# Kernel tuning notes

Hardware: AMD Instinct MI355X
Metric: run time of the kernel (lower is better)

Reference implementation:

```python
import jax, jax.numpy as jnp
import numpy as np

B, C, H, W = 64, 64, 64, 64
KD = 64  # kernel_dim == res == dim (required by the torch reshapes)


def _ln(t, g, b, eps=1e-5):
    mu = jnp.mean(t, axis=-1, keepdims=True)
    var = jnp.var(t, axis=-1, keepdims=True)
    return (t - mu) * jax.lax.rsqrt(var + eps) * g + b


def _cos_map(n, kd):
    i = jnp.arange(n, dtype=jnp.float32)[:, None]
    j = jnp.arange(kd, dtype=jnp.float32)[None, :]
    return jnp.cos(i * j * jnp.pi / n) / kd


def setup_inputs() -> dict:
    key = jax.random.key(0)
    ks = jax.random.split(key, 6)
    s = 0.02
    return {
        "x": jax.random.normal(ks[0], (B, C, H, W), jnp.float32),
        "freq_embed": jax.random.normal(ks[1], (H, W, C), jnp.float32),
        "g_k": jnp.ones((C,), jnp.float32), "b_k": jnp.zeros((C,), jnp.float32),
        "Wk": jax.random.normal(ks[2], (C, KD), jnp.float32) * s, "bk": jnp.zeros((KD,), jnp.float32),
        "g_z": jnp.ones((C,), jnp.float32), "b_z": jnp.zeros((C,), jnp.float32),
        "Wz": jax.random.normal(ks[3], (C, C), jnp.float32) * s, "bz": jnp.zeros((C,), jnp.float32),
        "g_o": jnp.ones((KD,), jnp.float32), "b_o": jnp.zeros((KD,), jnp.float32),
        "Wo": jax.random.normal(ks[4], (KD, C), jnp.float32) * s, "bo": jnp.zeros((C,), jnp.float32),
    }


def reference(x, freq_embed, g_k, b_k, Wk, bk, g_z, b_z, Wz, bz, g_o, b_o, Wo, bo):
    # x: (B,C,H,W) -> (B,H,W,C), matching the torch permute branch
    x = jnp.transpose(x, (0, 2, 3, 1))
    Bc, Hc, Wc, Cc = x.shape
    kd = Wk.shape[1]
    xin = x + freq_embed[None]                    # freq_embed broadcast over batch
    k = _ln(xin, g_k, b_k) @ Wk + bk              # (B,H,W,kd)
    z = _ln(freq_embed, g_z, b_z) @ Wz + bz       # to_k(freq_embed): (H,W,C)
    cosn = _cos_map(Hc, kd)                       # (H,kd)
    cosm = _cos_map(Wc, kd)                       # (W,kd)
    i = jnp.arange(Hc, dtype=jnp.float32)[:, None]
    j = jnp.arange(Wc, dtype=jnp.float32)[None, :]
    decay = (jnp.exp(-(i + j) / max(Hc, Wc)) / kd).astype(x.dtype)  # (H,W)
    wexp = decay[:, :, None] ** z                 # (H,W,C), decay > 0
    # separable forward DCT (two kernel-1 conv1d == two contractions)
    t = jnp.einsum('nh,bhwc->bnwc', cosn, k)
    t = jnp.einsum('mw,bnwc->bnmc', cosm, t)
    t = t * wexp[None]                            # exponential-decay spectral gate
    # separable inverse DCT
    t = jnp.einsum('nh,bnmc->bhmc', cosn, t)
    t = jnp.einsum('mw,bhmc->bhwc', cosm, t)
    out = _ln(t, g_o, b_o) * jax.nn.silu(z)[None]
    out = out @ Wo + bo
    return jnp.transpose(out, (0, 3, 1, 2))       # back to BCHW
```

## Files before the change

### kernel.cpp

```cpp
#include <hip/hip_runtime.h>


typedef __attribute__((ext_vector_type(8))) short short8;
typedef __attribute__((ext_vector_type(4))) float f32x4;
typedef __attribute__((ext_vector_type(4))) unsigned short us4;

__device__ __forceinline__ unsigned short bfhi(float f) {
    return (unsigned short)(__builtin_bit_cast(unsigned int, f) >> 16);
}
__device__ __forceinline__ float hif(float f) {
    return __builtin_bit_cast(float, __builtin_bit_cast(unsigned int, f) & 0xFFFF0000u);
}
__device__ __forceinline__ int swa(int row, int col) {
    return (row << 7) + (((col >> 3) ^ (row & 7)) << 4) + ((col & 7) << 1);
}
__device__ __forceinline__ short8 fragrd(const short* buf, int row, int kc) {
    int a = (row << 7) + ((kc ^ (row & 7)) << 4);
    return *(const short8*)((const char*)buf + a);
}

__device__ __forceinline__ void mm_block(const short* Ah, const short* Al,
                                         const short* Bh, const short* Bl,
                                         int m0, int n0, int l15, int q,
                                         f32x4 (&acc)[2][2]) {
    const f32x4 zero = {0.f, 0.f, 0.f, 0.f};
    acc[0][0] = zero; acc[0][1] = zero; acc[1][0] = zero; acc[1][1] = zero;
    #pragma unroll
    for (int kb = 0; kb < 2; ++kb) {
        int kc = (kb << 2) + q;
        short8 a0h = fragrd(Ah, m0 + l15, kc);
        short8 a0l = fragrd(Al, m0 + l15, kc);
        short8 a1h = fragrd(Ah, m0 + 16 + l15, kc);
        short8 a1l = fragrd(Al, m0 + 16 + l15, kc);
        short8 b0h = fragrd(Bh, n0 + l15, kc);
        short8 b0l = fragrd(Bl, n0 + l15, kc);
        short8 b1h = fragrd(Bh, n0 + 16 + l15, kc);
        short8 b1l = fragrd(Bl, n0 + 16 + l15, kc);
        acc[0][0] = __builtin_amdgcn_mfma_f32_16x16x32_bf16(a0h, b0h, acc[0][0], 0, 0, 0);
        acc[0][0] = __builtin_amdgcn_mfma_f32_16x16x32_bf16(a0h, b0l, acc[0][0], 0, 0, 0);
        acc[0][0] = __builtin_amdgcn_mfma_f32_16x16x32_bf16(a0l, b0h, acc[0][0], 0, 0, 0);
        acc[0][1] = __builtin_amdgcn_mfma_f32_16x16x32_bf16(a0h, b1h, acc[0][1], 0, 0, 0);
        acc[0][1] = __builtin_amdgcn_mfma_f32_16x16x32_bf16(a0h, b1l, acc[0][1], 0, 0, 0);
        acc[0][1] = __builtin_amdgcn_mfma_f32_16x16x32_bf16(a0l, b1h, acc[0][1], 0, 0, 0);
        acc[1][0] = __builtin_amdgcn_mfma_f32_16x16x32_bf16(a1h, b0h, acc[1][0], 0, 0, 0);
        acc[1][0] = __builtin_amdgcn_mfma_f32_16x16x32_bf16(a1h, b0l, acc[1][0], 0, 0, 0);
        acc[1][0] = __builtin_amdgcn_mfma_f32_16x16x32_bf16(a1l, b0h, acc[1][0], 0, 0, 0);
        acc[1][1] = __builtin_amdgcn_mfma_f32_16x16x32_bf16(a1h, b1h, acc[1][1], 0, 0, 0);
        acc[1][1] = __builtin_amdgcn_mfma_f32_16x16x32_bf16(a1h, b1l, acc[1][1], 0, 0, 0);
        acc[1][1] = __builtin_amdgcn_mfma_f32_16x16x32_bf16(a1l, b1h, acc[1][1], 0, 0, 0);
    }
}

__global__ __launch_bounds__(256) void k_pre1(
    const float* __restrict__ g_k, const float* __restrict__ b_k,
    const float* __restrict__ Wk, const float* __restrict__ bk,
    const float* __restrict__ g_z, const float* __restrict__ b_z,
    const float* __restrict__ Wz, const float* __restrict__ bz,
    const float* __restrict__ Wo,
    unsigned short* __restrict__ WkTh, unsigned short* __restrict__ WkTl,
    float* __restrict__ su_k, float* __restrict__ v_k,
    unsigned short* __restrict__ WzTh, unsigned short* __restrict__ WzTl,
    float* __restrict__ su_z, float* __restrict__ v_z,
    unsigned short* __restrict__ WoTh, unsigned short* __restrict__ WoTl,
    unsigned short* __restrict__ cos_hi, unsigned short* __restrict__ cos_lo) {
    int t = threadIdx.x;
    if (blockIdx.x < 16) {
        int n = blockIdx.x * 4 + (t >> 6);
        int c = t & 63;
        float wk = Wk[c * 64 + n];
        float a = g_k[c] * wk;
        WkTh[n * 64 + c] = bfhi(a);
        WkTl[n * 64 + c] = bfhi(a - hif(a));
        float sa = a, sv = b_k[c] * wk;
        #pragma unroll
        for (int off = 32; off > 0; off >>= 1) {
            sa += __shfl_xor(sa, off, 64);
            sv += __shfl_xor(sv, off, 64);
        }
        if (c == 0) { su_k[n] = sa; v_k[n] = sv + bk[n]; }
        float wz = Wz[c * 64 + n];
        float az = g_z[c] * wz;
        WzTh[n * 64 + c] = bfhi(az);
        WzTl[n * 64 + c] = bfhi(az - hif(az));
        float saz = az, svz = b_z[c] * wz;
        #pragma unroll
        for (int off = 32; off > 0; off >>= 1) {
            saz += __shfl_xor(saz, off, 64);
            svz += __shfl_xor(svz, off, 64);
        }
        if (c == 0) { su_z[n] = saz; v_z[n] = svz + bz[n]; }
        float wo = Wo[c * 64 + n];
        WoTh[n * 64 + c] = bfhi(wo);
        WoTl[n * 64 + c] = bfhi(wo - hif(wo));
    } else {
        int idx = (blockIdx.x - 16) * 256 + t;
        int i = idx >> 6, j = idx & 63;
        float ang = (float)(i * j) * 3.14159265358979323846f * (1.0f / 64.0f);
        float v = cosf(ang) * (1.0f / 64.0f);
        cos_hi[idx] = bfhi(v);
        cos_lo[idx] = bfhi(v - hif(v));
    }
}

__global__ __launch_bounds__(256) void k_pre2(
    const float* __restrict__ freq,
    const unsigned short* __restrict__ WzTh_g, const unsigned short* __restrict__ WzTl_g,
    const float* __restrict__ su_z, const float* __restrict__ v_z,
    float* __restrict__ siluzT, float* __restrict__ wexpT,
    float* __restrict__ freqT) {
    __shared__ short Ah[4096], Al[4096], Bh[4096], Bl[4096];
    __shared__ float muS[64], rsS[64];
    __shared__ float tile[64][65];
    int t = threadIdx.x;
    if (blockIdx.x < 64) {
        int h = blockIdx.x;
        #pragma unroll
        for (int p = 0; p < 2; ++p) {
            int e = t + p * 256;
            int row = e >> 3, ch = e & 7;
            int a = (row << 7) + (((ch ^ (row & 7)) << 4));
            *(uint4*)((char*)Bh + a) = *(const uint4*)&WzTh_g[row * 64 + ch * 8];
            *(uint4*)((char*)Bl + a) = *(const uint4*)&WzTl_g[row * 64 + ch * 8];
        }
        int w = t >> 2, c0 = (t & 3) << 4;
        float4 fr[4];
        float s1 = 0.f, s2 = 0.f;
        #pragma unroll
        for (int i = 0; i < 4; ++i) {
            fr[i] = *(const float4*)&freq[(h * 64 + w) * 64 + c0 + 4 * i];
            s1 += fr[i].x + fr[i].y + fr[i].z + fr[i].w;
            s2 += fr[i].x * fr[i].x + fr[i].y * fr[i].y + fr[i].z * fr[i].z + fr[i].w * fr[i].w;
        }
        s1 += __shfl_xor(s1, 1, 64); s1 += __shfl_xor(s1, 2, 64);
        s2 += __shfl_xor(s2, 1, 64); s2 += __shfl_xor(s2, 2, 64);
        float mu = s1 * (1.0f / 64.0f);
        float var = s2 * (1.0f / 64.0f) - mu * mu;
        float rs = rsqrtf(var + 1e-5f);
        if ((t & 3) == 0) { muS[w] = mu; rsS[w] = rs; }
        const float* fp = (const float*)fr;
        #pragma unroll
        for (int i = 0; i < 4; ++i) {
            us4 hv, lv;
            #pragma unroll
            for (int r = 0; r < 4; ++r) {
                float f = fp[i * 4 + r];
                hv[r] = bfhi(f);
                lv[r] = bfhi(f - hif(f));
            }
            int a = swa(w, c0 + 4 * i);
            *(us4*)((char*)Ah + a) = hv;
            *(us4*)((char*)Al + a) = lv;
        }
        __syncthreads();
        int lane = t & 63, wv = t >> 6;
        int q = lane >> 4, l15 = lane & 15;
        int m0 = (wv & 1) << 5, n0 = (wv >> 1) << 5;
        f32x4 acc[2][2];
        mm_block(Ah, Al, Bh, Bl, m0, n0, l15, q, acc);
        #pragma unroll
        for (int u = 0; u < 2; ++u) {
            int c = n0 + (u << 4) + l15;
            float suc = su_z[c], vc = v_z[c];
            #pragma unroll
            for (int ti = 0; ti < 2; ++ti) {
                int wb = m0 + (ti << 4) + (q << 2);
                float4 mu4 = *(const float4*)&muS[wb];
                float4 rs4 = *(const float4*)&rsS[wb];
                float4 sil, wx;
                #pragma unroll
                for (int r = 0; r < 4; ++r) {
                    float z = ((const float*)&rs4)[r] * (acc[ti][u][r] - ((const float*)&mu4)[r] * suc) + vc;
                    float lnd = -(float)(h + wb + r) * 0.015625f - 4.1588830833596718565f;
                    ((float*)&sil)[r] = z / (1.0f + expf(-z));
                    ((float*)&wx)[r] = expf(z * lnd);
                }
                int base = (c * 64 + h) * 64 + wb;
                *(float4*)&siluzT[base] = sil;
                *(float4*)&wexpT[base] = wx;
            }
        }
    } else {
        int h = blockIdx.x - 64;
        int w = t >> 2, c0 = (t & 3) << 4;
        #pragma unroll
        for (int i = 0; i < 4; ++i)
            *(float4*)&tile[w][c0 + 4 * i] = *(const float4*)&freq[(h * 64 + w) * 64 + c0 + 4 * i];
        __syncthreads();
        int w0 = (t & 15) << 2;
        #pragma unroll
        for (int p = 0; p < 4; ++p) {
            int c = (t >> 4) + 16 * p;
            float4 fv = make_float4(tile[w0][c], tile[w0 + 1][c], tile[w0 + 2][c], tile[w0 + 3][c]);
            *(float4*)&freqT[(c * 64 + h) * 64 + w0] = fv;
        }
    }
}

__global__ __launch_bounds__(256, 3) void k_k(
    const float* __restrict__ x, const float* __restrict__ freqT,
    const unsigned short* __restrict__ WkTh_g, const unsigned short* __restrict__ WkTl_g,
    const float* __restrict__ su_k, const float* __restrict__ v_k,
    float* __restrict__ planes) {
    __shared__ short Ah[4096], Al[4096], Bh[4096], Bl[4096];
    __shared__ __align__(16) float red1[16][68], red2[16][68];
    __shared__ float muS[64], rsS[64];
    int b = blockIdx.x >> 6, h = blockIdx.x & 63;
    int t = threadIdx.x;
    #pragma unroll
    for (int p = 0; p < 2; ++p) {
        int e = t + p * 256;
        int row = e >> 3, ch = e & 7;
        int a = (row << 7) + (((ch ^ (row & 7)) << 4));
        *(uint4*)((char*)Bh + a) = *(const uint4*)&WkTh_g[row * 64 + ch * 8];
        *(uint4*)((char*)Bl + a) = *(const uint4*)&WkTl_g[row * 64 + ch * 8];
    }
    int g = t >> 4, w0 = (t & 15) << 2, c0 = g << 2;
    const float* xb = x + (size_t)b * 262144 + h * 64;
    float4 vr[4];
    float4 s1 = {0,0,0,0}, s2 = {0,0,0,0};
    #pragma unroll
    for (int i = 0; i < 4; ++i) {
        int c = c0 + i;
        float4 xv = *(const float4*)&xb[c * 4096 + w0];
        float4 fv = *(const float4*)&freqT[c * 4096 + h * 64 + w0];
        xv.x += fv.x; xv.y += fv.y; xv.z += fv.z; xv.w += fv.w;
        vr[i] = xv;
        s1.x += xv.x; s1.y += xv.y; s1.z += xv.z; s1.w += xv.w;
        s2.x += xv.x * xv.x; s2.y += xv.y * xv.y; s2.z += xv.z * xv.z; s2.w += xv.w * xv.w;
    }
    const float* vp = (const float*)vr;
    #pragma unroll
    for (int j = 0; j < 4; ++j) {
        us4 hv, lv;
        #pragma unroll
        for (int r = 0; r < 4; ++r) {
            float f = vp[r * 4 + j];
            hv[r] = bfhi(f);
            lv[r] = bfhi(f - hif(f));
        }
        int a = swa(w0 + j, c0);
        *(us4*)((char*)Ah + a) = hv;
        *(us4*)((char*)Al + a) = lv;
    }
    *(float4*)&red1[g][w0] = s1;
    *(float4*)&red2[g][w0] = s2;
    __syncthreads();
    if (t < 64) {
        float a1 = 0.f, a2 = 0.f;
        #pragma unroll
        for (int j = 0; j < 16; ++j) { a1 += red1[j][t]; a2 += red2[j][t]; }
        float mu = a1 * (1.0f / 64.0f);
        float var = a2 * (1.0f / 64.0f) - mu * mu;
        muS[t] = mu; rsS[t] = rsqrtf(var + 1e-5f);
    }
    __syncthreads();
    int lane = t & 63, wv = t >> 6;
    int q = lane >> 4, l15 = lane & 15;
    int m0 = (wv & 1) << 5, n0 = (wv >> 1) << 5;
    f32x4 acc[2][2];
    mm_block(Ah, Al, Bh, Bl, m0, n0, l15, q, acc);
    #pragma unroll
    for (int u = 0; u < 2; ++u) {
        int n = n0 + (u << 4) + l15;
        float sun = su_k[n], vn = v_k[n];
        #pragma unroll
        for (int ti = 0; ti < 2; ++ti) {
            int wb = m0 + (ti << 4) + (q << 2);
            float4 mu4 = *(const float4*)&muS[wb];
            float4 rs4 = *(const float4*)&rsS[wb];
            float4 o;
            o.x = rs4.x * (acc[ti][u][0] - mu4.x * sun) + vn;
            o.y = rs4.y * (acc[ti][u][1] - mu4.y * sun) + vn;
            o.z = rs4.z * (acc[ti][u][2] - mu4.z * sun) + vn;
            o.w = rs4.w * (acc[ti][u][3] - mu4.w * sun) + vn;
            *(float4*)&planes[((size_t)(b * 64 + n) * 64 + h) * 64 + wb] = o;
        }
    }
}

__global__ __launch_bounds__(256, 3) void k_spec(
    float* __restrict__ planes,
    const unsigned short* __restrict__ cos_hi, const unsigned short* __restrict__ cos_lo,
    const float* __restrict__ wexpT) {
    __shared__ short Ch[4096], Cl[4096];
    __shared__ short D0h[4096], D0l[4096];
    __shared__ short D1h[4096], D1l[4096];
    int b = blockIdx.x >> 6, c = blockIdx.x & 63;
    float* po = planes + (size_t)(b * 64 + c) * 4096;
    int t = threadIdx.x;
    int lane = t & 63, wv = t >> 6;
    int q = lane >> 4, l15 = lane & 15;
    int m0 = (wv & 1) << 5, n0 = (wv >> 1) << 5;

    {
        int r = t >> 2, cb = (t & 3) << 4;
        #pragma unroll
        for (int p = 0; p < 2; ++p) {
            int chunk = (cb >> 3) + p;
            int a = (r << 7) + (((chunk ^ (r & 7)) << 4));
            *(uint4*)((char*)Ch + a) = *(const uint4*)&cos_hi[r * 64 + cb + p * 8];
            *(uint4*)((char*)Cl + a) = *(const uint4*)&cos_lo[r * 64 + cb + p * 8];
        }
    }
    {
        int w = t & 63, h0 = (t >> 6) << 4;
        float v[16];
        #pragma unroll
        for (int j = 0; j < 16; ++j) v[j] = po[(h0 + j) * 64 + w];
        #pragma unroll
        for (int g = 0; g < 4; ++g) {
            int col = h0 + (g << 2);
            int a = swa(w, col);
            us4 hv, lv;
            #pragma unroll
            for (int r = 0; r < 4; ++r) {
                float f = v[(g << 2) + r];
                hv[r] = bfhi(f);
                lv[r] = bfhi(f - hif(f));
            }
            *(us4*)((char*)D0h + a) = hv;
            *(us4*)((char*)D0l + a) = lv;
        }
    }
    __syncthreads();

    f32x4 acc[2][2];

#define WB_T(Dh, Dl)                                                                \
    {                                                                               \
        _Pragma("unroll")                                                           \
        for (int ti = 0; ti < 2; ++ti)                                              \
            _Pragma("unroll")                                                       \
            for (int u = 0; u < 2; ++u) {                                           \
                int row = n0 + (u << 4) + l15;                                      \
                int col = m0 + (ti << 4) + (q << 2);                                \
                int a = swa(row, col);                                              \
                us4 hv, lv;                                                         \
                _Pragma("unroll")                                                   \
                for (int r = 0; r < 4; ++r) {                                       \
                    float f = acc[ti][u][r];                                        \
                    hv[r] = bfhi(f);                                                \
                    lv[r] = bfhi(f - hif(f));                                       \
                }                                                                   \
                *(us4*)((char*)Dh + a) = hv;                                        \
                *(us4*)((char*)Dl + a) = lv;                                        \
            }                                                                       \
    }

    mm_block(D0h, D0l, Ch, Cl, m0, n0, l15, q, acc);
    WB_T(D1h, D1l)
    __syncthreads();
    mm_block(D1h, D1l, Ch, Cl, m0, n0, l15, q, acc);
    {
        const float* wx = wexpT + (size_t)c * 4096;
        #pragma unroll
        for (int ti = 0; ti < 2; ++ti)
            #pragma unroll
            for (int u = 0; u < 2; ++u)
                #pragma unroll
                for (int r = 0; r < 4; ++r) {
                    int n = m0 + (ti << 4) + (q << 2) + r;
                    int m = n0 + (u << 4) + l15;
                    acc[ti][u][r] *= wx[n * 64 + m];
                }
    }
    WB_T(D0h, D0l)
    __syncthreads();
    mm_block(Ch, Cl, D0h, D0l, m0, n0, l15, q, acc);
    {
        #pragma unroll
        for (int ti = 0; ti < 2; ++ti)
            #pragma unroll
            for (int u = 0; u < 2; ++u)
                #pragma unroll
                for (int r = 0; r < 4; ++r) {
                    int row = m0 + (ti << 4) + (q << 2) + r;
                    int col = n0 + (u << 4) + l15;
                    int a = swa(row, col);
                    float f = acc[ti][u][r];
                    *(unsigned short*)((char*)D1h + a) = bfhi(f);
                    *(unsigned short*)((char*)D1l + a) = bfhi(f - hif(f));
                }
    }
    __syncthreads();
    mm_block(D1h, D1l, Ch, Cl, m0, n0, l15, q, acc);
    {
        #pragma unroll
        for (int ti = 0; ti < 2; ++ti)
            #pragma unroll
            for (int u = 0; u < 2; ++u)
                #pragma unroll
                for (int r = 0; r < 4; ++r) {
                    int h = m0 + (ti << 4) + (q << 2) + r;
                    int w = n0 + (u << 4) + l15;
                    po[h * 64 + w] = acc[ti][u][r];
                }
    }
#undef WB_T
}

__global__ __launch_bounds__(256, 3) void k_out(
    const float* __restrict__ planes, const float* __restrict__ siluzT,
    const float* __restrict__ g_o, const float* __restrict__ b_o,
    const unsigned short* __restrict__ WoTh_g, const unsigned short* __restrict__ WoTl_g,
    const float* __restrict__ bo, float* __restrict__ out) {
    __shared__ short Ah[4096], Al[4096], Bh[4096], Bl[4096];
    __shared__ __align__(16) float red1[16][68], red2[16][68];
    __shared__ float muS[64], rsS[64];
    int b = blockIdx.x >> 6, h = blockIdx.x & 63;
    int t = threadIdx.x;
    #pragma unroll
    for (int p = 0; p < 2; ++p) {
        int e = t + p * 256;
        int row = e >> 3, ch = e & 7;
        int a = (row << 7) + (((ch ^ (row & 7)) << 4));
        *(uint4*)((char*)Bh + a) = *(const uint4*)&WoTh_g[row * 64 + ch * 8];
        *(uint4*)((char*)Bl + a) = *(const uint4*)&WoTl_g[row * 64 + ch * 8];
    }
    int g = t >> 4, w0 = (t & 15) << 2, c0 = g << 2;
    const float* pb = planes + (size_t)b * 262144 + h * 64;
    float4 vr[4], szr[4];
    float4 s1 = {0,0,0,0}, s2 = {0,0,0,0};
    #pragma unroll
    for (int i = 0; i < 4; ++i) {
        int c = c0 + i;
        float4 tv = *(const float4*)&pb[c * 4096 + w0];
        szr[i] = *(const float4*)&siluzT[c * 4096 + h * 64 + w0];
        vr[i] = tv;
        s1.x += tv.x; s1.y += tv.y; s1.z += tv.z; s1.w += tv.w;
        s2.x += tv.x * tv.x; s2.y += tv.y * tv.y; s2.z += tv.z * tv.z; s2.w += tv.w * tv.w;
    }
    *(float4*)&red1[g][w0] = s1;
    *(float4*)&red2[g][w0] = s2;
    __syncthreads();
    if (t < 64) {
        float a1 = 0.f, a2 = 0.f;
        #pragma unroll
        for (int j = 0; j < 16; ++j) { a1 += red1[j][t]; a2 += red2[j][t]; }
        float mu = a1 * (1.0f / 64.0f);
        float var = a2 * (1.0f / 64.0f) - mu * mu;
        muS[t] = mu; rsS[t] = rsqrtf(var + 1e-5f);
    }
    __syncthreads();
    {
        float4 mu4 = *(const float4*)&muS[w0];
        float4 rs4 = *(const float4*)&rsS[w0];
        #pragma unroll
        for (int i = 0; i < 4; ++i) {
            int c = c0 + i;
            float go = g_o[c], boc = b_o[c];
            vr[i].x = ((vr[i].x - mu4.x) * rs4.x * go + boc) * szr[i].x;
            vr[i].y = ((vr[i].y - mu4.y) * rs4.y * go + boc) * szr[i].y;
            vr[i].z = ((vr[i].z - mu4.z) * rs4.z * go + boc) * szr[i].z;
            vr[i].w = ((vr[i].w - mu4.w) * rs4.w * go + boc) * szr[i].w;
        }
        const float* vp = (const float*)vr;
        #pragma unroll
        for (int j = 0; j < 4; ++j) {
            us4 hv, lv;
            #pragma unroll
            for (int r = 0; r < 4; ++r) {
                float f = vp[r * 4 + j];
                hv[r] = bfhi(f);
                lv[r] = bfhi(f - hif(f));
            }
            int a = swa(w0 + j, c0);
            *(us4*)((char*)Ah + a) = hv;
            *(us4*)((char*)Al + a) = lv;
        }
    }
    __syncthreads();
    int lane = t & 63, wv = t >> 6;
    int q = lane >> 4, l15 = lane & 15;
    int m0 = (wv & 1) << 5, n0 = (wv >> 1) << 5;
    f32x4 acc[2][2];
    mm_block(Ah, Al, Bh, Bl, m0, n0, l15, q, acc);
    #pragma unroll
    for (int u = 0; u < 2; ++u) {
        int o_ = n0 + (u << 4) + l15;
        float bov = bo[o_];
        #pragma unroll
        for (int ti = 0; ti < 2; ++ti) {
            int wb = m0 + (ti << 4) + (q << 2);
            float4 o;
            o.x = acc[ti][u][0] + bov;
            o.y = acc[ti][u][1] + bov;
            o.z = acc[ti][u][2] + bov;
            o.w = acc[ti][u][3] + bov;
            *(float4*)&out[((size_t)(b * 64 + o_) * 64 + h) * 64 + wb] = o;
        }
    }
}

extern "C" void kernel_launch(void* const* d_in, const int* in_sizes, int n_in,
                              void* d_out, int out_size, void* d_ws, size_t ws_size,
                              hipStream_t stream) {
    const float* x    = (const float*)d_in[0];
    const float* freq = (const float*)d_in[1];
    const float* g_k  = (const float*)d_in[2];
    const float* b_k  = (const float*)d_in[3];
    const float* Wk   = (const float*)d_in[4];
    const float* bk   = (const float*)d_in[5];
    const float* g_z  = (const float*)d_in[6];
    const float* b_z  = (const float*)d_in[7];
    const float* Wz   = (const float*)d_in[8];
    const float* bz   = (const float*)d_in[9];
    const float* g_o  = (const float*)d_in[10];
    const float* b_o  = (const float*)d_in[11];
    const float* Wo   = (const float*)d_in[12];
    const float* bo   = (const float*)d_in[13];
    float* out = (float*)d_out;

    float* ws = (float*)d_ws;
    float* planes = ws;
    float* siluzT = planes + 16777216;
    float* wexpT  = siluzT + 262144;
    float* freqT  = wexpT + 262144;
    float* su_k   = freqT + 262144;
    float* v_k    = su_k + 64;
    float* su_z   = v_k + 64;
    float* v_z    = su_z + 64;
    unsigned short* cos_hi = (unsigned short*)(v_z + 64);
    unsigned short* cos_lo = cos_hi + 4096;
    unsigned short* WkTh = cos_lo + 4096;
    unsigned short* WkTl = WkTh + 4096;
    unsigned short* WzTh = WkTl + 4096;
    unsigned short* WzTl = WzTh + 4096;
    unsigned short* WoTh = WzTl + 4096;
    unsigned short* WoTl = WoTh + 4096;

    k_pre1<<<32, 256, 0, stream>>>(g_k, b_k, Wk, bk, g_z, b_z, Wz, bz, Wo,
                                   WkTh, WkTl, su_k, v_k, WzTh, WzTl, su_z, v_z,
                                   WoTh, WoTl, cos_hi, cos_lo);
    k_pre2<<<128, 256, 0, stream>>>(freq, WzTh, WzTl, su_z, v_z, siluzT, wexpT, freqT);
    k_k<<<4096, 256, 0, stream>>>(x, freqT, WkTh, WkTl, su_k, v_k, planes);
    k_spec<<<4096, 256, 0, stream>>>(planes, cos_hi, cos_lo, wexpT);
    k_out<<<4096, 256, 0, stream>>>(planes, siluzT, g_o, b_o, WoTh, WoTl, bo, out);
}
```

Measured before the change: 212.0 us.

## Give each wave its own DCT plane and keep weight fragments in registers

k_spec is restructured so that each 64-thread wave processes one full 64x64 plane. The cosine matrix fragments stay in registers, the intermediate stays in a per-wave LDS buffer, and the block-level __syncthreads are gone. The launch becomes 2048 blocks of 128 threads. k_k and k_out now load the weight B-fragments straight from global memory into registers instead of staging them in LDS, and they reduce the LayerNorm statistics with wave shuffles, which frees LDS and allows a higher occupancy hint. The cost is much heavier register pressure in k_spec (many short8 fragments live at once), which could spill or reduce occupancy.

```diff
diff --git a/kernel.cpp b/kernel.cpp
--- a/kernel.cpp
+++ b/kernel.cpp
@@ -17,6 +17,12 @@
 __device__ __forceinline__ short8 fragrd(const short* buf, int row, int kc) {
     int a = (row << 7) + ((kc ^ (row & 7)) << 4);
     return *(const short8*)((const char*)buf + a);
+}
+__device__ __forceinline__ f32x4 mm3(short8 ah, short8 al, short8 bh, short8 bl, f32x4 acc) {
+    acc = __builtin_amdgcn_mfma_f32_16x16x32_bf16(ah, bh, acc, 0, 0, 0);
+    acc = __builtin_amdgcn_mfma_f32_16x16x32_bf16(ah, bl, acc, 0, 0, 0);
+    acc = __builtin_amdgcn_mfma_f32_16x16x32_bf16(al, bh, acc, 0, 0, 0);
+    return acc;
 }
 
 __device__ __forceinline__ void mm_block(const short* Ah, const short* Al,
@@ -36,18 +42,31 @@
         short8 b0l = fragrd(Bl, n0 + l15, kc);
         short8 b1h = fragrd(Bh, n0 + 16 + l15, kc);
         short8 b1l = fragrd(Bl, n0 + 16 + l15, kc);
-        acc[0][0] = __builtin_amdgcn_mfma_f32_16x16x32_bf16(a0h, b0h, acc[0][0], 0, 0, 0);
-        acc[0][0] = __builtin_amdgcn_mfma_f32_16x16x32_bf16(a0h, b0l, acc[0][0], 0, 0, 0);
-        acc[0][0] = __builtin_amdgcn_mfma_f32_16x16x32_bf16(a0l, b0h, acc[0][0], 0, 0, 0);
-        acc[0][1] = __builtin_amdgcn_mfma_f32_16x16x32_bf16(a0h, b1h, acc[0][1], 0, 0, 0);
-        acc[0][1] = __builtin_amdgcn_mfma_f32_16x16x32_bf16(a0h, b1l, acc[0][1], 0, 0, 0);
-        acc[0][1] = __builtin_amdgcn_mfma_f32_16x16x32_bf16(a0l, b1h, acc[0][1], 0, 0, 0);
-        acc[1][0] = __builtin_amdgcn_mfma_f32_16x16x32_bf16(a1h, b0h, acc[1][0], 0, 0, 0);
-        acc[1][0] = __builtin_amdgcn_mfma_f32_16x16x32_bf16(a1h, b0l, acc[1][0], 0, 0, 0);
-        acc[1][0] = __builtin_amdgcn_mfma_f32_16x16x32_bf16(a1l, b0h, acc[1][0], 0, 0, 0);
-        acc[1][1] = __builtin_amdgcn_mfma_f32_16x16x32_bf16(a1h, b1h, acc[1][1], 0, 0, 0);
-        acc[1][1] = __builtin_amdgcn_mfma_f32_16x16x32_bf16(a1h, b1l, acc[1][1], 0, 0, 0);
-        acc[1][1] = __builtin_amdgcn_mfma_f32_16x16x32_bf16(a1l, b1h, acc[1][1], 0, 0, 0);
+        acc[0][0] = mm3(a0h, a0l, b0h, b0l, acc[0][0]);
+        acc[0][1] = mm3(a0h, a0l, b1h, b1l, acc[0][1]);
+        acc[1][0] = mm3(a1h, a1l, b0h, b0l, acc[1][0]);
+        acc[1][1] = mm3(a1h, a1l, b1h, b1l, acc[1][1]);
+    }
+}
+
+__device__ __forceinline__ void mm_block_regB(const short* Ah, const short* Al,
+                                              const short8 (&bf)[2][2][2],
+                                              int m0, int l15, int q,
+                                              f32x4 (&acc)[2][2]) {
+    const f32x4 zero = {0.f, 0.f, 0.f, 0.f};
+    acc[0][0] = zero; acc[0][1] = zero; acc[1][0] = zero; acc[1][1] = zero;
+    #pragma unroll
+    for (int kb = 0; kb < 2; ++kb) {
+        int kc = (kb << 2) + q;
+        short8 a0h = fragrd(Ah, m0 + l15, kc);
+        short8 a0l = fragrd(Al, m0 + l15, kc);
+        short8 a1h = fragrd(Ah, m0 + 16 + l15, kc);
+        short8 a1l = fragrd(Al, m0 + 16 + l15, kc);
+        #pragma unroll
+        for (int u = 0; u < 2; ++u) {
+            acc[0][u] = mm3(a0h, a0l, bf[u][kb][0], bf[u][kb][1], acc[0][u]);
+            acc[1][u] = mm3(a1h, a1l, bf[u][kb][0], bf[u][kb][1], acc[1][u]);
+        }
     }
 }
 
@@ -108,7 +127,7 @@
     const float* __restrict__ su_z, const float* __restrict__ v_z,
     float* __restrict__ siluzT, float* __restrict__ wexpT,
     float* __restrict__ freqT) {
-    __shared__ short Ah[4096], Al[4096], Bh[4096], Bl[4096];
+    __shared__ __align__(16) short Ah[4096], Al[4096], Bh[4096], Bl[4096];
     __shared__ float muS[64], rsS[64];
     __shared__ float tile[64][65];
     int t = threadIdx.x;
@@ -196,39 +215,45 @@
     }
 }
 
-__global__ __launch_bounds__(256, 3) void k_k(
+__global__ __launch_bounds__(256, 4) void k_k(
     const float* __restrict__ x, const float* __restrict__ freqT,
     const unsigned short* __restrict__ WkTh_g, const unsigned short* __restrict__ WkTl_g,
     const float* __restrict__ su_k, const float* __restrict__ v_k,
     float* __restrict__ planes) {
-    __shared__ short Ah[4096], Al[4096], Bh[4096], Bl[4096];
-    __shared__ __align__(16) float red1[16][68], red2[16][68];
-    __shared__ float muS[64], rsS[64];
+    __shared__ __align__(16) short Ah[4096], Al[4096];
+    __shared__ __align__(16) float red1[4][64], red2[4][64];
+    __shared__ __align__(16) float muS[64], rsS[64];
     int b = blockIdx.x >> 6, h = blockIdx.x & 63;
     int t = threadIdx.x;
-    #pragma unroll
-    for (int p = 0; p < 2; ++p) {
-        int e = t + p * 256;
-        int row = e >> 3, ch = e & 7;
-        int a = (row << 7) + (((ch ^ (row & 7)) << 4));
-        *(uint4*)((char*)Bh + a) = *(const uint4*)&WkTh_g[row * 64 + ch * 8];
-        *(uint4*)((char*)Bl + a) = *(const uint4*)&WkTl_g[row * 64 + ch * 8];
-    }
+    int lane = t & 63, wv = t >> 6;
+    int q = lane >> 4, l15 = lane & 15;
+    int m0 = (wv & 1) << 5, n0 = (wv >> 1) << 5;
+    short8 bf[2][2][2];
+    #pragma unroll
+    for (int u = 0; u < 2; ++u)
+        #pragma unroll
+        for (int kb = 0; kb < 2; ++kb) {
+            int off = (n0 + (u << 4) + l15) * 64 + ((kb << 2) + q) * 8;
+            bf[u][kb][0] = *(const short8*)&WkTh_g[off];
+            bf[u][kb][1] = *(const short8*)&WkTl_g[off];
+        }
     int g = t >> 4, w0 = (t & 15) << 2, c0 = g << 2;
     const float* xb = x + (size_t)b * 262144 + h * 64;
-    float4 vr[4];
-    float4 s1 = {0,0,0,0}, s2 = {0,0,0,0};
+    float4 xv[4], fv[4];
     #pragma unroll
     for (int i = 0; i < 4; ++i) {
-        int c = c0 + i;
-        float4 xv = *(const float4*)&xb[c * 4096 + w0];
-        float4 fv = *(const float4*)&freqT[c * 4096 + h * 64 + w0];
-        xv.x += fv.x; xv.y += fv.y; xv.z += fv.z; xv.w += fv.w;
-        vr[i] = xv;
-        s1.x += xv.x; s1.y += xv.y; s1.z += xv.z; s1.w += xv.w;
-        s2.x += xv.x * xv.x; s2.y += xv.y * xv.y; s2.z += xv.z * xv.z; s2.w += xv.w * xv.w;
-    }
-    const float* vp = (const float*)vr;
+        xv[i] = *(const float4*)&xb[(c0 + i) * 4096 + w0];
+        fv[i] = *(const float4*)&freqT[(c0 + i) * 4096 + h * 64 + w0];
+    }
+    float4 s1 = {0, 0, 0, 0}, s2 = {0, 0, 0, 0};
+    #pragma unroll
+    for (int i = 0; i < 4; ++i) {
+        xv[i].x += fv[i].x; xv[i].y += fv[i].y; xv[i].z += fv[i].z; xv[i].w += fv[i].w;
+        s1.x += xv[i].x; s1.y += xv[i].y; s1.z += xv[i].z; s1.w += xv[i].w;
+        s2.x += xv[i].x * xv[i].x; s2.y += xv[i].y * xv[i].y;
+        s2.z += xv[i].z * xv[i].z; s2.w += xv[i].w * xv[i].w;
+    }
+    const float* vp = (const float*)xv;
     #pragma unroll
     for (int j = 0; j < 4; ++j) {
         us4 hv, lv;
@@ -242,23 +267,30 @@
         *(us4*)((char*)Ah + a) = hv;
         *(us4*)((char*)Al + a) = lv;
     }
-    *(float4*)&red1[g][w0] = s1;
-    *(float4*)&red2[g][w0] = s2;
+    #pragma unroll
+    for (int r = 0; r < 4; ++r) {
+        float a1 = ((const float*)&s1)[r];
+        float a2 = ((const float*)&s2)[r];
+        a1 += __shfl_xor(a1, 16, 64); a1 += __shfl_xor(a1, 32, 64);
+        a2 += __shfl_xor(a2, 16, 64); a2 += __shfl_xor(a2, 32, 64);
+        ((float*)&s1)[r] = a1;
+        ((float*)&s2)[r] = a2;
+    }
+    if (lane < 16) {
+        *(float4*)&red1[wv][lane << 2] = s1;
+        *(float4*)&red2[wv][lane << 2] = s2;
+    }
     __syncthreads();
     if (t < 64) {
-        float a1 = 0.f, a2 = 0.f;
-        #pragma unroll
-        for (int j = 0; j < 16; ++j) { a1 += red1[j][t]; a2 += red2[j][t]; }
+        float a1 = red1[0][t] + red1[1][t] + red1[2][t] + red1[3][t];
+        float a2 = red2[0][t] + red2[1][t] + red2[2][t] + red2[3][t];
         float mu = a1 * (1.0f / 64.0f);
         float var = a2 * (1.0f / 64.0f) - mu * mu;
         muS[t] = mu; rsS[t] = rsqrtf(var + 1e-5f);
     }
     __syncthreads();
-    int lane = t & 63, wv = t >> 6;
-    int q = lane >> 4, l15 = lane & 15;
-    int m0 = (wv & 1) << 5, n0 = (wv >> 1) << 5;
     f32x4 acc[2][2];
-    mm_block(Ah, Al, Bh, Bl, m0, n0, l15, q, acc);
+    mm_block_regB(Ah, Al, bf, m0, l15, q, acc);
     #pragma unroll
     for (int u = 0; u < 2; ++u) {
         int n = n0 + (u << 4) + l15;
@@ -278,165 +310,225 @@
     }
 }
 
-__global__ __launch_bounds__(256, 3) void k_spec(
+__global__ __launch_bounds__(128, 2) void k_spec(
     float* __restrict__ planes,
     const unsigned short* __restrict__ cos_hi, const unsigned short* __restrict__ cos_lo,
     const float* __restrict__ wexpT) {
-    __shared__ short Ch[4096], Cl[4096];
-    __shared__ short D0h[4096], D0l[4096];
-    __shared__ short D1h[4096], D1l[4096];
-    int b = blockIdx.x >> 6, c = blockIdx.x & 63;
-    float* po = planes + (size_t)(b * 64 + c) * 4096;
+    __shared__ __align__(16) short DhS[2][4096], DlS[2][4096];
+    int t = threadIdx.x;
+    int wv = t >> 6, lane = t & 63;
+    int q = lane >> 4, l15 = lane & 15;
+    int pid = blockIdx.x * 2 + wv;
+    int c = pid & 63;
+    float* po = planes + (size_t)pid * 4096;
+    const float* wx = wexpT + (size_t)c * 4096;
+    short* dh = DhS[wv];
+    short* dl = DlS[wv];
+
+    short8 cf[4][2][2];
+    #pragma unroll
+    for (int rg = 0; rg < 4; ++rg)
+        #pragma unroll
+        for (int kb = 0; kb < 2; ++kb) {
+            int off = (rg * 16 + l15) * 64 + ((kb << 2) + q) * 8;
+            cf[rg][kb][0] = *(const short8*)&cos_hi[off];
+            cf[rg][kb][1] = *(const short8*)&cos_lo[off];
+        }
+
+    #pragma unroll
+    for (int jg = 0; jg < 16; ++jg) {
+        float f0 = po[(jg * 4 + 0) * 64 + lane];
+        float f1 = po[(jg * 4 + 1) * 64 + lane];
+        float f2 = po[(jg * 4 + 2) * 64 + lane];
+        float f3 = po[(jg * 4 + 3) * 64 + lane];
+        us4 hv, lv;
+        hv[0] = bfhi(f0); lv[0] = bfhi(f0 - hif(f0));
+        hv[1] = bfhi(f1); lv[1] = bfhi(f1 - hif(f1));
+        hv[2] = bfhi(f2); lv[2] = bfhi(f2 - hif(f2));
+        hv[3] = bfhi(f3); lv[3] = bfhi(f3 - hif(f3));
+        int a = swa(lane, jg << 2);
+        *(us4*)((char*)dh + a) = hv;
+        *(us4*)((char*)dl + a) = lv;
+    }
+
+    short8 af[4][2][2];
+    f32x4 acc[2][2];
+    const f32x4 zacc = {0.f, 0.f, 0.f, 0.f};
+
+#define LOAD_AF()                                                            \
+    _Pragma("unroll")                                                        \
+    for (int rg = 0; rg < 4; ++rg) {                                         \
+        _Pragma("unroll")                                                    \
+        for (int kb = 0; kb < 2; ++kb) {                                     \
+            af[rg][kb][0] = fragrd(dh, rg * 16 + l15, (kb << 2) + q);        \
+            af[rg][kb][1] = fragrd(dl, rg * 16 + l15, (kb << 2) + q);        \
+        }                                                                    \
+    }
+
+#define QMM(ASRC, BSRC)                                                      \
+    acc[0][0] = zacc; acc[0][1] = zacc; acc[1][0] = zacc; acc[1][1] = zacc;  \
+    __builtin_amdgcn_s_setprio(1);                                           \
+    _Pragma("unroll")                                                        \
+    for (int kb = 0; kb < 2; ++kb)                                           \
+        _Pragma("unroll")                                                    \
+        for (int ti = 0; ti < 2; ++ti)                                       \
+            _Pragma("unroll")                                                \
+            for (int u = 0; u < 2; ++u)                                      \
+                acc[ti][u] = mm3(ASRC[2 * mq + ti][kb][0], ASRC[2 * mq + ti][kb][1], \
+                                 BSRC[2 * nq + u][kb][0], BSRC[2 * nq + u][kb][1],   \
+                                 acc[ti][u]);                                \
+    __builtin_amdgcn_s_setprio(0);
+
+#define WB_T()                                                               \
+    _Pragma("unroll")                                                        \
+    for (int ti = 0; ti < 2; ++ti)                                           \
+        _Pragma("unroll")                                                    \
+        for (int u = 0; u < 2; ++u) {                                        \
+            int row = (nq << 5) + (u << 4) + l15;                            \
+            int col = (mq << 5) + (ti << 4) + (q << 2);                      \
+            int a = swa(row, col);                                           \
+            us4 hv, lv;                                                      \
+            _Pragma("unroll")                                                \
+            for (int r = 0; r < 4; ++r) {                                    \
+                float f = acc[ti][u][r];                                     \
+                hv[r] = bfhi(f);                                             \
+                lv[r] = bfhi(f - hif(f));                                    \
+            }                                                                \
+            *(us4*)((char*)dh + a) = hv;                                     \
+            *(us4*)((char*)dl + a) = lv;                                     \
+        }
+
+    LOAD_AF()
+    #pragma unroll
+    for (int mq = 0; mq < 2; ++mq)
+        #pragma unroll
+        for (int nq = 0; nq < 2; ++nq) {
+            QMM(af, cf)
+            WB_T()
+        }
+
+    LOAD_AF()
+    #pragma unroll
+    for (int mq = 0; mq < 2; ++mq)
+        #pragma unroll
+        for (int nq = 0; nq < 2; ++nq) {
+            float wxr[2][2][4];
+            #pragma unroll
+            for (int ti = 0; ti < 2; ++ti)
+                #pragma unroll
+                for (int u = 0; u < 2; ++u)
+                    #pragma unroll
+                    for (int r = 0; r < 4; ++r)
+                        wxr[ti][u][r] = wx[((mq << 5) + (ti << 4) + (q << 2) + r) * 64
+                                           + (nq << 5) + (u << 4) + l15];
+            QMM(af, cf)
+            #pragma unroll
+            for (int ti = 0; ti < 2; ++ti)
+                #pragma unroll
+                for (int u = 0; u < 2; ++u)
+                    #pragma unroll
+                    for (int r = 0; r < 4; ++r)
+                        acc[ti][u][r] *= wxr[ti][u][r];
+            WB_T()
+        }
+
+    LOAD_AF()
+    #pragma unroll
+    for (int mq = 0; mq < 2; ++mq)
+        #pragma unroll
+        for (int nq = 0; nq < 2; ++nq) {
+            QMM(cf, af)
+            #pragma unroll
+            for (int ti = 0; ti < 2; ++ti)
+                #pragma unroll
+                for (int u = 0; u < 2; ++u)
+                    #pragma unroll
+                    for (int r = 0; r < 4; ++r) {
+                        int row = (mq << 5) + (ti << 4) + (q << 2) + r;
+                        int col = (nq << 5) + (u << 4) + l15;
+                        int a = swa(row, col);
+                        float f = acc[ti][u][r];
+                        *(unsigned short*)((char*)dh + a) = bfhi(f);
+                        *(unsigned short*)((char*)dl + a) = bfhi(f - hif(f));
+                    }
+        }
+
+    LOAD_AF()
+    #pragma unroll
+    for (int mq = 0; mq < 2; ++mq)
+        #pragma unroll
+        for (int nq = 0; nq < 2; ++nq) {
+            QMM(af, cf)
+            #pragma unroll
+            for (int ti = 0; ti < 2; ++ti)
+                #pragma unroll
+                for (int u = 0; u < 2; ++u)
+                    #pragma unroll
+                    for (int r = 0; r < 4; ++r) {
+                        int h = (mq << 5) + (ti << 4) + (q << 2) + r;
+                        int w = (nq << 5) + (u << 4) + l15;
+                        po[h * 64 + w] = acc[ti][u][r];
+                    }
+        }
+#undef LOAD_AF
+#undef QMM
+#undef WB_T
+}
+
+__global__ __launch_bounds__(256, 4) void k_out(
+    const float* __restrict__ planes, const float* __restrict__ siluzT,
+    const float* __restrict__ g_o, const float* __restrict__ b_o,
+    const unsigned short* __restrict__ WoTh_g, const unsigned short* __restrict__ WoTl_g,
+    const float* __restrict__ bo, float* __restrict__ out) {
+    __shared__ __align__(16) short Ah[4096], Al[4096];
+    __shared__ __align__(16) float red1[4][64], red2[4][64];
+    __shared__ __align__(16) float muS[64], rsS[64];
+    int b = blockIdx.x >> 6, h = blockIdx.x & 63;
     int t = threadIdx.x;
     int lane = t & 63, wv = t >> 6;
     int q = lane >> 4, l15 = lane & 15;
     int m0 = (wv & 1) << 5, n0 = (wv >> 1) << 5;
-
-    {
-        int r = t >> 2, cb = (t & 3) << 4;
-        #pragma unroll
-        for (int p = 0; p < 2; ++p) {
-            int chunk = (cb >> 3) + p;
-            int a = (r << 7) + (((chunk ^ (r & 7)) << 4));
-            *(uint4*)((char*)Ch + a) = *(const uint4*)&cos_hi[r * 64 + cb + p * 8];
-            *(uint4*)((char*)Cl + a) = *(const uint4*)&cos_lo[r * 64 + cb + p * 8];
-        }
-    }
-    {
-        int w = t & 63, h0 = (t >> 6) << 4;
-        float v[16];
-        #pragma unroll
-        for (int j = 0; j < 16; ++j) v[j] = po[(h0 + j) * 64 + w];
-        #pragma unroll
-        for (int g = 0; g < 4; ++g) {
-            int col = h0 + (g << 2);
-            int a = swa(w, col);
-            us4 hv, lv;
-            #pragma unroll
-            for (int r = 0; r < 4; ++r) {
-                float f = v[(g << 2) + r];
-                hv[r] = bfhi(f);
-                lv[r] = bfhi(f - hif(f));
-            }
-            *(us4*)((char*)D0h + a) = hv;
-            *(us4*)((char*)D0l + a) = lv;
-        }
-    }
-    __syncthreads();
-
-    f32x4 acc[2][2];
-
-#define WB_T(Dh, Dl)                                                                \
-    {                                                                               \
-        _Pragma("unroll")                                                           \
-        for (int ti = 0; ti < 2; ++ti)                                              \
-            _Pragma("unroll")                                                       \
-            for (int u = 0; u < 2; ++u) {                                           \
-                int row = n0 + (u << 4) + l15;                                      \
-                int col = m0 + (ti << 4) + (q << 2);                                \
-                int a = swa(row, col);                                              \
-                us4 hv, lv;                                                         \
-                _Pragma("unroll")                                                   \
-                for (int r = 0; r < 4; ++r) {                                       \
-                    float f = acc[ti][u][r];                                        \
-                    hv[r] = bfhi(f);                                                \
-                    lv[r] = bfhi(f - hif(f));                                       \
-                }                                                                   \
-                *(us4*)((char*)Dh + a) = hv;                                        \
-                *(us4*)((char*)Dl + a) = lv;                                        \
-            }                                                                       \
-    }
-
-    mm_block(D0h, D0l, Ch, Cl, m0, n0, l15, q, acc);
-    WB_T(D1h, D1l)
-    __syncthreads();
-    mm_block(D1h, D1l, Ch, Cl, m0, n0, l15, q, acc);
-    {
-        const float* wx = wexpT + (size_t)c * 4096;
-        #pragma unroll
-        for (int ti = 0; ti < 2; ++ti)
-            #pragma unroll
-            for (int u = 0; u < 2; ++u)
-                #pragma unroll
-                for (int r = 0; r < 4; ++r) {
-                    int n = m0 + (ti << 4) + (q << 2) + r;
-                    int m = n0 + (u << 4) + l15;
-                    acc[ti][u][r] *= wx[n * 64 + m];
-                }
-    }
-    WB_T(D0h, D0l)
-    __syncthreads();
-    mm_block(Ch, Cl, D0h, D0l, m0, n0, l15, q, acc);
-    {
-        #pragma unroll
-        for (int ti = 0; ti < 2; ++ti)
-            #pragma unroll
-            for (int u = 0; u < 2; ++u)
-                #pragma unroll
-                for (int r = 0; r < 4; ++r) {
-                    int row = m0 + (ti << 4) + (q << 2) + r;
-                    int col = n0 + (u << 4) + l15;
-                    int a = swa(row, col);
-                    float f = acc[ti][u][r];
-                    *(unsigned short*)((char*)D1h + a) = bfhi(f);
-                    *(unsigned short*)((char*)D1l + a) = bfhi(f - hif(f));
-                }
-    }
-    __syncthreads();
-    mm_block(D1h, D1l, Ch, Cl, m0, n0, l15, q, acc);
-    {
-        #pragma unroll
-        for (int ti = 0; ti < 2; ++ti)
-            #pragma unroll
-            for (int u = 0; u < 2; ++u)
-                #pragma unroll
-                for (int r = 0; r < 4; ++r) {
-                    int h = m0 + (ti << 4) + (q << 2) + r;
-                    int w = n0 + (u << 4) + l15;
-                    po[h * 64 + w] = acc[ti][u][r];
-                }
-    }
-#undef WB_T
-}
-
-__global__ __launch_bounds__(256, 3) void k_out(
-    const float* __restrict__ planes, const float* __restrict__ siluzT,
-    const float* __restrict__ g_o, const float* __restrict__ b_o,
-    const unsigned short* __restrict__ WoTh_g, const unsigned short* __restrict__ WoTl_g,
-    const float* __restrict__ bo, float* __restrict__ out) {
-    __shared__ short Ah[4096], Al[4096], Bh[4096], Bl[4096];
-    __shared__ __align__(16) float red1[16][68], red2[16][68];
-    __shared__ float muS[64], rsS[64];
-    int b = blockIdx.x >> 6, h = blockIdx.x & 63;
-    int t = threadIdx.x;
-    #pragma unroll
-    for (int p = 0; p < 2; ++p) {
-        int e = t + p * 256;
-        int row = e >> 3, ch = e & 7;
-        int a = (row << 7) + (((ch ^ (row & 7)) << 4));
-        *(uint4*)((char*)Bh + a) = *(const uint4*)&WoTh_g[row * 64 + ch * 8];
-        *(uint4*)((char*)Bl + a) = *(const uint4*)&WoTl_g[row * 64 + ch * 8];
-    }
+    short8 bf[2][2][2];
+    #pragma unroll
+    for (int u = 0; u < 2; ++u)
+        #pragma unroll
+        for (int kb = 0; kb < 2; ++kb) {
+            int off = (n0 + (u << 4) + l15) * 64 + ((kb << 2) + q) * 8;
+            bf[u][kb][0] = *(const short8*)&WoTh_g[off];
+            bf[u][kb][1] = *(const short8*)&WoTl_g[off];
+        }
     int g = t >> 4, w0 = (t & 15) << 2, c0 = g << 2;
     const float* pb = planes + (size_t)b * 262144 + h * 64;
     float4 vr[4], szr[4];
-    float4 s1 = {0,0,0,0}, s2 = {0,0,0,0};
     #pragma unroll
     for (int i = 0; i < 4; ++i) {
-        int c = c0 + i;
-        float4 tv = *(const float4*)&pb[c * 4096 + w0];
-        szr[i] = *(const float4*)&siluzT[c * 4096 + h * 64 + w0];
-        vr[i] = tv;
-        s1.x += tv.x; s1.y += tv.y; s1.z += tv.z; s1.w += tv.w;
-        s2.x += tv.x * tv.x; s2.y += tv.y * tv.y; s2.z += tv.z * tv.z; s2.w += tv.w * tv.w;
-    }
-    *(float4*)&red1[g][w0] = s1;
-    *(float4*)&red2[g][w0] = s2;
+        vr[i] = *(const float4*)&pb[(c0 + i) * 4096 + w0];
+        szr[i] = *(const float4*)&siluzT[(c0 + i) * 4096 + h * 64 + w0];
+    }
+    float4 s1 = {0, 0, 0, 0}, s2 = {0, 0, 0, 0};
+    #pragma unroll
+    for (int i = 0; i < 4; ++i) {
+        s1.x += vr[i].x; s1.y += vr[i].y; s1.z += vr[i].z; s1.w += vr[i].w;
+        s2.x += vr[i].x * vr[i].x; s2.y += vr[i].y * vr[i].y;
+        s2.z += vr[i].z * vr[i].z; s2.w += vr[i].w * vr[i].w;
+    }
+    #pragma unroll
+    for (int r = 0; r < 4; ++r) {
+        float a1 = ((const float*)&s1)[r];
+        float a2 = ((const float*)&s2)[r];
+        a1 += __shfl_xor(a1, 16, 64); a1 += __shfl_xor(a1, 32, 64);
+        a2 += __shfl_xor(a2, 16, 64); a2 += __shfl_xor(a2, 32, 64);
+        ((float*)&s1)[r] = a1;
+        ((float*)&s2)[r] = a2;
+    }
+    if (lane < 16) {
+        *(float4*)&red1[wv][lane << 2] = s1;
+        *(float4*)&red2[wv][lane << 2] = s2;
+    }
     __syncthreads();
     if (t < 64) {
-        float a1 = 0.f, a2 = 0.f;
-        #pragma unroll
-        for (int j = 0; j < 16; ++j) { a1 += red1[j][t]; a2 += red2[j][t]; }
+        float a1 = red1[0][t] + red1[1][t] + red1[2][t] + red1[3][t];
+        float a2 = red2[0][t] + red2[1][t] + red2[2][t] + red2[3][t];
         float mu = a1 * (1.0f / 64.0f);
         float var = a2 * (1.0f / 64.0f) - mu * mu;
         muS[t] = mu; rsS[t] = rsqrtf(var + 1e-5f);
@@ -447,8 +539,8 @@
         float4 rs4 = *(const float4*)&rsS[w0];
         #pragma unroll
         for (int i = 0; i < 4; ++i) {
-            int c = c0 + i;
-            float go = g_o[c], boc = b_o[c];
+            int cc = c0 + i;
+            float go = g_o[cc], boc = b_o[cc];
             vr[i].x = ((vr[i].x - mu4.x) * rs4.x * go + boc) * szr[i].x;
             vr[i].y = ((vr[i].y - mu4.y) * rs4.y * go + boc) * szr[i].y;
             vr[i].z = ((vr[i].z - mu4.z) * rs4.z * go + boc) * szr[i].z;
@@ -470,11 +562,8 @@
         }
     }
     __syncthreads();
-    int lane = t & 63, wv = t >> 6;
-    int q = lane >> 4, l15 = lane & 15;
-    int m0 = (wv & 1) << 5, n0 = (wv >> 1) << 5;
     f32x4 acc[2][2];
-    mm_block(Ah, Al, Bh, Bl, m0, n0, l15, q, acc);
+    mm_block_regB(Ah, Al, bf, m0, l15, q, acc);
     #pragma unroll
     for (int u = 0; u < 2; ++u) {
         int o_ = n0 + (u << 4) + l15;
@@ -534,6 +623,6 @@
                                    WoTh, WoTl, cos_hi, cos_lo);
     k_pre2<<<128, 256, 0, stream>>>(freq, WzTh, WzTl, su_z, v_z, siluzT, wexpT, freqT);
     k_k<<<4096, 256, 0, stream>>>(x, freqT, WkTh, WkTl, su_k, v_k, planes);
-    k_spec<<<4096, 256, 0, stream>>>(planes, cos_hi, cos_lo, wexpT);
+    k_spec<<<2048, 128, 0, stream>>>(planes, cos_hi, cos_lo, wexpT);
     k_out<<<4096, 256, 0, stream>>>(planes, siluzT, g_o, b_o, WoTh, WoTl, bo, out);
 }
```

Measured after the change: 230.7 us. 1.09x slower.
